# Optimization experiments

Measured on AMD Instinct MI355X. Metric: run time of the kernel, lower is better.

The kernel has to match this reference:

```python
import jax, jax.numpy as jnp
import numpy as np

NUM_HEADS = 10
LN_EPS = 1e-5


def setup_inputs() -> dict:
    key = jax.random.key(0)
    ks = jax.random.split(key, 6)
    N, D = 4096, 640  # in_dim == out_dim required by residual add
    x = jax.random.normal(ks[0], (N, D), dtype=jnp.float32)
    s = 1.0 / np.sqrt(D)
    Wq = jax.random.normal(ks[1], (D, D), dtype=jnp.float32) * s  # torch Linear weight [out,in]
    Wk = jax.random.normal(ks[2], (D, D), dtype=jnp.float32) * s
    Wv = jax.random.normal(ks[3], (D, D), dtype=jnp.float32) * s
    gamma = jnp.ones((D,), dtype=jnp.float32)
    beta = jnp.zeros((D,), dtype=jnp.float32)
    return {"x": x, "Wq": Wq, "Wk": Wk, "Wv": Wv, "gamma": gamma, "beta": beta}


def reference(x, Wq, Wk, Wv, gamma, beta):
    N, D = x.shape
    dk = D // NUM_HEADS
    Q = x @ Wq.T  # [N, D]
    K = x @ Wk.T
    V = x @ Wv.T
    # Faithful to source: raw reshapes (NOT transposes)
    Qh = Q.reshape(NUM_HEADS, N, dk)
    Kh = K.reshape(NUM_HEADS, N, dk).reshape(NUM_HEADS, dk, N)  # torch.reshape, not .mT
    Vh = V.reshape(NUM_HEADS, N, dk)
    # Faithful quirk: scale by sqrt(K.shape[2]) == sqrt(N)
    scale = np.float32(np.sqrt(N))
    wghts = jax.nn.softmax((Qh @ Kh) / scale, axis=-1)  # [H, N, N]
    values = wghts @ Vh  # [H, N, dk]
    values = values.reshape(N, NUM_HEADS * dk)  # raw reshape merge
    values = values + x  # residual
    # LayerNorm(out_dim), biased variance, eps=1e-5
    mean = jnp.mean(values, axis=-1, keepdims=True)
    var = jnp.mean(jnp.square(values - mean), axis=-1, keepdims=True)
    out = (values - mean) * jax.lax.rsqrt(var + LN_EPS) * gamma + beta
    return out
```

## Files before the change

### kernel.cpp

```cpp
#include <hip/hip_runtime.h>
#if __has_include(<hip/hip_fp8.h>)
#include <hip/hip_fp8.h>
#endif


typedef __bf16 bf16x8 __attribute__((ext_vector_type(8)));
typedef __bf16 bf16x4 __attribute__((ext_vector_type(4)));
typedef float  f32x4  __attribute__((ext_vector_type(4)));
typedef unsigned short u16x4 __attribute__((ext_vector_type(4)));
typedef unsigned int   u32x4 __attribute__((ext_vector_type(4)));
typedef long           la64  __attribute__((may_alias));
typedef unsigned int   ua32  __attribute__((may_alias));

#define N_TOK   4096
#define D_MODEL 640
#define DK      64
#define HSLAB   (N_TOK * DK)
#define SQS 0.15014030f

#if __has_builtin(__builtin_amdgcn_exp2f)
#define EXP2(x) __builtin_amdgcn_exp2f(x)
#else
#define EXP2(x) exp2f(x)
#endif

__device__ __forceinline__ void stage16(const void* g, void* lds_uniform) {
    __builtin_amdgcn_global_load_lds(
        (const __attribute__((address_space(1))) unsigned int*)g,
        (__attribute__((address_space(3))) unsigned int*)lds_uniform, 16, 0, 0);
}

__device__ __forceinline__ u16x4 cvt4(f32x4 v) {
    return __builtin_bit_cast(u16x4, __builtin_convertvector(v, bf16x4));
}

__device__ __forceinline__ unsigned int pk_fp8(f32x4 v) {
#if __has_builtin(__builtin_amdgcn_cvt_pk_fp8_f32)
    int r = 0;
    r = __builtin_amdgcn_cvt_pk_fp8_f32(v[0], v[1], r, false);
    r = __builtin_amdgcn_cvt_pk_fp8_f32(v[2], v[3], r, true);
    return (unsigned int)r;
#else
    union { unsigned char b[4]; unsigned int u; } x;
    x.b[0] = __hip_fp8_e4m3(v[0]).__x;
    x.b[1] = __hip_fp8_e4m3(v[1]).__x;
    x.b[2] = __hip_fp8_e4m3(v[2]).__x;
    x.b[3] = __hip_fp8_e4m3(v[3]).__x;
    return x.u;
#endif
}

__global__ __launch_bounds__(256) void cvt_all(const float* __restrict__ x,
                                               const float* __restrict__ w0,
                                               const float* __restrict__ w1,
                                               const float* __restrict__ w2,
                                               unsigned short* __restrict__ xb,
                                               unsigned short* __restrict__ d0,
                                               unsigned short* __restrict__ d1,
                                               unsigned short* __restrict__ d2,
                                               f32x4* __restrict__ ltot4) {
    int i = blockIdx.x * 256 + threadIdx.x;
    if (i >= 962560) { ltot4[i - 962560] = (f32x4){0.f, 0.f, 0.f, 0.f}; return; }
    const float* s; unsigned short* d; int off; float scl = 1.0f;
    if (i < 655360) { s = x; d = xb; off = i; }
    else {
        int j = i - 655360;
        int w = j / 102400; off = j - w * 102400;
        s = (w == 0) ? w0 : (w == 1) ? w1 : w2;
        d = (w == 0) ? d0 : (w == 1) ? d1 : d2;
        if (w < 2) scl = SQS;
    }
    f32x4 v = ((const f32x4*)s)[off];
    v[0] *= scl; v[1] *= scl; v[2] *= scl; v[3] *= scl;
    ((u16x4*)d)[off] = cvt4(v);
}

__global__ __launch_bounds__(256, 2) void gemm_qkv(
    const unsigned short* __restrict__ xb,
    const unsigned short* __restrict__ wq,
    const unsigned short* __restrict__ wk,
    const unsigned short* __restrict__ wv,
    unsigned short* __restrict__ Qo,
    unsigned short* __restrict__ Ko,
    unsigned short* __restrict__ Vo) {
    const int mode = blockIdx.z;
    const unsigned short* W = (mode == 0) ? wq : (mode == 1) ? wk : wv;
    unsigned short*       C = (mode == 0) ? Qo : (mode == 1) ? Ko : Vo;
    const int m0 = blockIdx.y * 128;
    const int n0 = blockIdx.x * 128;

    __shared__ unsigned short As[8192];
    __shared__ unsigned short Bs[8192];

    const int tid  = threadIdx.x;
    const int lane = tid & 63;
    const int wave = tid >> 6;
    const int quad = lane >> 4, l16 = lane & 15;
    const int wm = (wave >> 1) * 64, wn = (wave & 1) * 64;
    const int swz = l16 & 7;

    f32x4 acc[4][4] = {};

    int prow[4], pcol[4], lbase[4];
    for (int j = 0; j < 4; j++) {
        int p = j * 256 + tid;
        prow[j] = p >> 3;
        pcol[j] = ((p & 7) ^ (prow[j] & 7)) * 8;
        lbase[j] = (j * 256 + wave * 64) * 8;
    }

    for (int kt = 0; kt < D_MODEL; kt += 64) {
        __syncthreads();
        for (int j = 0; j < 4; j++) {
            stage16(&xb[(size_t)(m0 + prow[j]) * D_MODEL + kt + pcol[j]], As + lbase[j]);
            stage16(&W [(size_t)(n0 + prow[j]) * D_MODEL + kt + pcol[j]], Bs + lbase[j]);
        }
        __syncthreads();

        for (int s = 0; s < 2; s++) {
            bf16x8 af[4], bfr[4];
            for (int mi = 0; mi < 4; mi++) {
                int row = wm + mi * 16 + l16;
                af[mi] = *(const bf16x8*)&As[row * 64 + (((s << 2) + quad) ^ swz) * 8];
            }
            for (int ni = 0; ni < 4; ni++) {
                int row = wn + ni * 16 + l16;
                bfr[ni] = *(const bf16x8*)&Bs[row * 64 + (((s << 2) + quad) ^ swz) * 8];
            }
            for (int mi = 0; mi < 4; mi++)
                for (int ni = 0; ni < 4; ni++)
                    acc[mi][ni] = __builtin_amdgcn_mfma_f32_16x16x32_bf16(af[mi], bfr[ni], acc[mi][ni], 0, 0, 0);
        }
    }

    for (int mi = 0; mi < 4; mi++)
        for (int ni = 0; ni < 4; ni++) {
            u16x4 cv = cvt4(acc[mi][ni]);
            for (int r = 0; r < 4; r++) {
                int row = m0 + wm + mi * 16 + quad * 4 + r;
                int col = n0 + wn + ni * 16 + l16;
                C[(size_t)row * D_MODEL + col] = cv[r];
            }
        }
}

__global__ __launch_bounds__(256) void transpose_kv(
    const unsigned short* __restrict__ Kn, unsigned char* __restrict__ Kp8,
    const unsigned short* __restrict__ Vn, unsigned char* __restrict__ Vp8,
    const unsigned short* __restrict__ Qn, unsigned char* __restrict__ Qf8) {
    const int z = blockIdx.z;
    const int t = threadIdx.x;

    if (z >= 20) {
        const size_t base = (size_t)(z - 20) * HSLAB + blockIdx.x * 4096 + t * 16;
        bf16x8 v0 = *(const bf16x8*)&Qn[base];
        bf16x8 v1 = *(const bf16x8*)&Qn[base + 8];
        f32x4 a = {(float)v0[0], (float)v0[1], (float)v0[2], (float)v0[3]};
        f32x4 b = {(float)v0[4], (float)v0[5], (float)v0[6], (float)v0[7]};
        f32x4 c = {(float)v1[0], (float)v1[1], (float)v1[2], (float)v1[3]};
        f32x4 d = {(float)v1[4], (float)v1[5], (float)v1[6], (float)v1[7]};
        u32x4 o = {pk_fp8(a), pk_fp8(b), pk_fp8(c), pk_fp8(d)};
        *(u32x4*)&Qf8[base] = o;
        return;
    }

    __shared__ unsigned short T[64][66];
    const unsigned short* src; unsigned char* dst;
    int R, Cc, r0, c0;
    if (z < 10) { src = Kn; dst = Kp8; R = 64;   Cc = 4096; r0 = 0; c0 = blockIdx.x * 64; }
    else        { src = Vn; dst = Vp8; R = 4096; Cc = 64;   r0 = blockIdx.x * 64; c0 = 0; }
    const size_t hb = (size_t)(z % 10) * HSLAB;
    const int rr = t >> 3, c8 = (t & 7) * 8;

    for (int hf = 0; hf < 2; hf++) {
        int r = rr + hf * 32;
        bf16x8 v = *(const bf16x8*)&src[hb + (size_t)(r0 + r) * Cc + c0 + c8];
        for (int j = 0; j < 8; j++) T[r][c8 + j] = ((unsigned short*)&v)[j];
    }
    __syncthreads();
    const bf16x8 zz = {};
    for (int hf = 0; hf < 2; hf++) {
        int r = rr + hf * 32;
        *(bf16x8*)&((unsigned short*)src)[hb + (size_t)(r0 + r) * Cc + c0 + c8] = zz;
    }
    for (int hf = 0; hf < 2; hf++) {
        int oc = rr + hf * 32;
        f32x4 lo, hi;
        for (int j = 0; j < 4; j++) {
            lo[j] = __builtin_bit_cast(float, (unsigned int)T[c8 + j][oc] << 16);
            hi[j] = __builtin_bit_cast(float, (unsigned int)T[c8 + 4 + j][oc] << 16);
        }
        uint2 ov; ov.x = pk_fp8(lo); ov.y = pk_fp8(hi);
        size_t dcol = (z < 10) ? ((size_t)(c0 + oc) * 64 + r0 + c8)
                               : ((size_t)oc * 4096 + r0 + c8);
        *(uint2*)&dst[hb + dcol] = ov;
    }
}

__global__ __launch_bounds__(256, 4) void attn(
    const unsigned char* __restrict__ Qf8,
    const unsigned char* __restrict__ Kp8,
    const unsigned char* __restrict__ Vp8,
    float* __restrict__ vals,
    float* __restrict__ l_tot) {
    const int h  = blockIdx.x >> 5;
    const int qt = blockIdx.x & 31;
    const int ntile = (blockIdx.y == 2) ? 10 : 11;
    const int tile0 = blockIdx.y * 11;
    const int lane = threadIdx.x & 63;
    const int wave = threadIdx.x >> 6;
    const int quad = lane >> 4, l16 = lane & 15;
    const size_t hoff = (size_t)h * HSLAB;

    __shared__ unsigned char sm[32768];
    unsigned char* Kt = sm;
    unsigned char* Vt = sm + 8192;
    unsigned char* Pw = sm + 16384 + wave * 4096;

    const int qbase = qt * 128 + wave * 32;
    long qd[2][2];
    for (int g = 0; g < 2; g++) {
        const unsigned char* qp = Qf8 + hoff + (size_t)(qbase + g * 16 + l16) * 64 + quad * 8;
        qd[g][0] = *(const la64*)(qp);
        qd[g][1] = *(const la64*)(qp + 32);
    }

    f32x4 o[2][4] = {};
    f32x4 ol[2] = {};
    const long ONES8 = 0x3838383838383838L;

    const int cA = wave * 64 + lane, cB = cA + 256;
    const int kKeyA = ((cA >> 5) << 3) + (cA & 7), kCiA = (cA >> 3) & 3;
    const int kKeyB = ((cB >> 5) << 3) + (cB & 7), kCiB = (cB >> 3) & 3;
    const int vDkA  = ((cA >> 6) << 3) + (cA & 7), vCvA = (cA >> 3) & 7;
    const int vDkB  = ((cB >> 6) << 3) + (cB & 7), vCvB = (cB >> 3) & 7;

    const int kfb = (l16 >> 3) * 512 + (quad >> 1) * 128 + (l16 & 7) * 16 + (quad & 1) * 8;
    const int vfb = (l16 >> 3) * 1024 + (quad >> 1) * 128 + (l16 & 7) * 16 + (quad & 1) * 8;

    for (int t = 0; t < ntile; t++) {
        const int keyb = (tile0 + t) << 7;
        __syncthreads();
        stage16(Kp8 + hoff + (size_t)(keyb + kKeyA) * 64 + kCiA * 16, Kt + wave * 1024);
        stage16(Kp8 + hoff + (size_t)(keyb + kKeyB) * 64 + kCiB * 16, Kt + 4096 + wave * 1024);
        stage16(Vp8 + hoff + (size_t)vDkA * N_TOK + keyb + vCvA * 16, Vt + wave * 1024);
        stage16(Vp8 + hoff + (size_t)vDkB * N_TOK + keyb + vCvB * 16, Vt + 4096 + wave * 1024);
        __syncthreads();

        for (int ni = 0; ni < 8; ni++) {
            const unsigned char* kp = Kt + ni * 1024 + kfb;
            long a0 = *(const la64*)(kp);
            long a1 = *(const la64*)(kp + 256);
            for (int g = 0; g < 2; g++) {
                f32x4 s = {};
                s = __builtin_amdgcn_mfma_f32_16x16x32_fp8_fp8(a0, qd[g][0], s, 0, 0, 0);
                s = __builtin_amdgcn_mfma_f32_16x16x32_fp8_fp8(a1, qd[g][1], s, 0, 0, 0);
                f32x4 pv;
                for (int r = 0; r < 4; r++) pv[r] = EXP2(s[r]);
                *(ua32*)(Pw + (ni * 2 + (quad >> 1)) * 256 +
                         (g * 16 + l16) * 8 + (quad & 1) * 4) = pk_fp8(pv);
            }
        }

        __syncthreads();

        for (int ks = 0; ks < 4; ks++) {
            long vf[4];
            for (int nd = 0; nd < 4; nd++)
                vf[nd] = *(const la64*)(Vt + nd * 2048 + ks * 256 + vfb);
            for (int g = 0; g < 2; g++) {
                long pf = *(const la64*)(Pw + (ks * 4 + quad) * 256 + (g * 16 + l16) * 8);
                ol[g] = __builtin_amdgcn_mfma_f32_16x16x32_fp8_fp8(pf, ONES8, ol[g], 0, 0, 0);
                for (int nd = 0; nd < 4; nd++)
                    o[g][nd] = __builtin_amdgcn_mfma_f32_16x16x32_fp8_fp8(pf, vf[nd], o[g][nd], 0, 0, 0);
            }
        }
    }

    if (l16 == 0)
        for (int g = 0; g < 2; g++)
            for (int r = 0; r < 4; r++)
                atomicAdd(&l_tot[(h << 12) + qbase + g * 16 + quad * 4 + r], ol[g][r]);

    for (int g = 0; g < 2; g++)
        for (int nd = 0; nd < 4; nd++)
            for (int r = 0; r < 4; r++) {
                int q = qbase + g * 16 + quad * 4 + r;
                atomicAdd(&vals[hoff + (size_t)q * DK + nd * 16 + l16], o[g][nd][r]);
            }
}

__global__ __launch_bounds__(256) void ln_kernel(
    const float* __restrict__ vals, const float* __restrict__ l_tot,
    const float* __restrict__ x,
    const float* __restrict__ gamma, const float* __restrict__ beta,
    float* __restrict__ out) {
    const int wave = threadIdx.x >> 6, lane = threadIdx.x & 63;
    const int row  = blockIdx.x * 4 + wave;
    const float* v  = vals + (size_t)row * D_MODEL;
    const float* xr = x    + (size_t)row * D_MODEL;

    float t[10];
    float s = 0.f;
    for (int i = 0; i < 10; i++) {
        float linv = 1.0f / l_tot[row * 10 + i];
        t[i] = v[lane + i * 64] * linv + xr[lane + i * 64];
        s += t[i];
    }
    for (int off = 32; off; off >>= 1) s += __shfl_xor(s, off, 64);
    float mean = s * (1.0f / 640.0f);
    float s2 = 0.f;
    for (int i = 0; i < 10; i++) { float d = t[i] - mean; s2 += d * d; }
    for (int off = 32; off; off >>= 1) s2 += __shfl_xor(s2, off, 64);
    float inv = rsqrtf(s2 * (1.0f / 640.0f) + 1e-5f);

    float* orow = out + (size_t)row * D_MODEL;
    for (int i = 0; i < 10; i++) {
        int c = lane + i * 64;
        orow[c] = (t[i] - mean) * inv * gamma[c] + beta[c];
    }
}

extern "C" void kernel_launch(void* const* d_in, const int* in_sizes, int n_in,
                              void* d_out, int out_size, void* d_ws, size_t ws_size,
                              hipStream_t stream) {
    const float* x     = (const float*)d_in[0];
    const float* Wq    = (const float*)d_in[1];
    const float* Wk    = (const float*)d_in[2];
    const float* Wv    = (const float*)d_in[3];
    const float* gamma = (const float*)d_in[4];
    const float* beta  = (const float*)d_in[5];
    float* out = (float*)d_out;

    char* ws = (char*)d_ws;
    unsigned short* xb  = (unsigned short*)(ws);
    unsigned char*  Qf8 = (unsigned char*)(ws);
    unsigned short* wqb = (unsigned short*)(ws + 5242880);
    unsigned short* wkb = (unsigned short*)(ws + 6062080);
    unsigned short* wvb = (unsigned short*)(ws + 6881280);
    unsigned short* Qn  = (unsigned short*)(ws + 7700480);
    unsigned char*  Kp8 = (unsigned char*)(ws + 12943360);
    unsigned char*  Vp8 = (unsigned char*)(ws + 18186240);
    unsigned short* Kn  = (unsigned short*)(ws + 23429120);
    unsigned short* Vn  = (unsigned short*)(ws + 28672000);
    float*          vals  = (float*)(ws + 23429120);
    float*          l_tot = (float*)(ws + 33914880);

    cvt_all<<<3800, 256, 0, stream>>>(x, Wq, Wk, Wv, xb, wqb, wkb, wvb,
                                      (f32x4*)l_tot);

    gemm_qkv<<<dim3(5, 32, 3), 256, 0, stream>>>(xb, wqb, wkb, wvb, Qn, Kn, Vn);

    transpose_kv<<<dim3(64, 1, 30), 256, 0, stream>>>(Kn, Kp8, Vn, Vp8, Qn, Qf8);

    attn<<<dim3(320, 3), 256, 0, stream>>>(Qf8, Kp8, Vp8, vals, l_tot);
    ln_kernel<<<1024, 256, 0, stream>>>(vals, l_tot, x, gamma, beta, out);
}
```

Measured before the change: 160.2 us.

## Keep P in registers and use bf16 PV MFMA, fusing Q fp8 conversion into attention

```diff
diff --git a/kernel.cpp b/kernel.cpp
--- a/kernel.cpp
+++ b/kernel.cpp
@@ -8,9 +8,8 @@
 typedef __bf16 bf16x4 __attribute__((ext_vector_type(4)));
 typedef float  f32x4  __attribute__((ext_vector_type(4)));
 typedef unsigned short u16x4 __attribute__((ext_vector_type(4)));
-typedef unsigned int   u32x4 __attribute__((ext_vector_type(4)));
+typedef short          s16x4 __attribute__((ext_vector_type(4)));
 typedef long           la64  __attribute__((may_alias));
-typedef unsigned int   ua32  __attribute__((may_alias));
 
 #define N_TOK   4096
 #define D_MODEL 640
@@ -48,6 +47,10 @@
     x.b[3] = __hip_fp8_e4m3(v[3]).__x;
     return x.u;
 #endif
+}
+
+__device__ __forceinline__ f32x4 mfma16bf(s16x4 a, s16x4 b, f32x4 c) {
+    return __builtin_amdgcn_mfma_f32_16x16x16bf16_1k(a, b, c, 0, 0, 0);
 }
 
 __global__ __launch_bounds__(256) void cvt_all(const float* __restrict__ x,
@@ -146,29 +149,15 @@
 
 __global__ __launch_bounds__(256) void transpose_kv(
     const unsigned short* __restrict__ Kn, unsigned char* __restrict__ Kp8,
-    const unsigned short* __restrict__ Vn, unsigned char* __restrict__ Vp8,
-    const unsigned short* __restrict__ Qn, unsigned char* __restrict__ Qf8) {
+    const unsigned short* __restrict__ Vn, unsigned short* __restrict__ Vpb) {
     const int z = blockIdx.z;
     const int t = threadIdx.x;
 
-    if (z >= 20) {
-        const size_t base = (size_t)(z - 20) * HSLAB + blockIdx.x * 4096 + t * 16;
-        bf16x8 v0 = *(const bf16x8*)&Qn[base];
-        bf16x8 v1 = *(const bf16x8*)&Qn[base + 8];
-        f32x4 a = {(float)v0[0], (float)v0[1], (float)v0[2], (float)v0[3]};
-        f32x4 b = {(float)v0[4], (float)v0[5], (float)v0[6], (float)v0[7]};
-        f32x4 c = {(float)v1[0], (float)v1[1], (float)v1[2], (float)v1[3]};
-        f32x4 d = {(float)v1[4], (float)v1[5], (float)v1[6], (float)v1[7]};
-        u32x4 o = {pk_fp8(a), pk_fp8(b), pk_fp8(c), pk_fp8(d)};
-        *(u32x4*)&Qf8[base] = o;
-        return;
-    }
-
     __shared__ unsigned short T[64][66];
-    const unsigned short* src; unsigned char* dst;
-    int R, Cc, r0, c0;
-    if (z < 10) { src = Kn; dst = Kp8; R = 64;   Cc = 4096; r0 = 0; c0 = blockIdx.x * 64; }
-    else        { src = Vn; dst = Vp8; R = 4096; Cc = 64;   r0 = blockIdx.x * 64; c0 = 0; }
+    const unsigned short* src;
+    int Cc, r0, c0;
+    if (z < 10) { src = Kn; Cc = 4096; r0 = 0; c0 = blockIdx.x * 64; }
+    else        { src = Vn; Cc = 64;   r0 = blockIdx.x * 64; c0 = 0; }
     const size_t hb = (size_t)(z % 10) * HSLAB;
     const int rr = t >> 3, c8 = (t & 7) * 8;
 
@@ -183,24 +172,31 @@
         int r = rr + hf * 32;
         *(bf16x8*)&((unsigned short*)src)[hb + (size_t)(r0 + r) * Cc + c0 + c8] = zz;
     }
-    for (int hf = 0; hf < 2; hf++) {
-        int oc = rr + hf * 32;
-        f32x4 lo, hi;
-        for (int j = 0; j < 4; j++) {
-            lo[j] = __builtin_bit_cast(float, (unsigned int)T[c8 + j][oc] << 16);
-            hi[j] = __builtin_bit_cast(float, (unsigned int)T[c8 + 4 + j][oc] << 16);
-        }
-        uint2 ov; ov.x = pk_fp8(lo); ov.y = pk_fp8(hi);
-        size_t dcol = (z < 10) ? ((size_t)(c0 + oc) * 64 + r0 + c8)
-                               : ((size_t)oc * 4096 + r0 + c8);
-        *(uint2*)&dst[hb + dcol] = ov;
-    }
-}
-
-__global__ __launch_bounds__(256, 4) void attn(
-    const unsigned char* __restrict__ Qf8,
-    const unsigned char* __restrict__ Kp8,
-    const unsigned char* __restrict__ Vp8,
+    if (z < 10) {
+        for (int hf = 0; hf < 2; hf++) {
+            int oc = rr + hf * 32;
+            f32x4 lo, hi;
+            for (int j = 0; j < 4; j++) {
+                lo[j] = __builtin_bit_cast(float, (unsigned int)T[c8 + j][oc] << 16);
+                hi[j] = __builtin_bit_cast(float, (unsigned int)T[c8 + 4 + j][oc] << 16);
+            }
+            uint2 ov; ov.x = pk_fp8(lo); ov.y = pk_fp8(hi);
+            *(uint2*)&Kp8[hb + (size_t)(c0 + oc) * 64 + r0 + c8] = ov;
+        }
+    } else {
+        for (int hf = 0; hf < 2; hf++) {
+            int oc = rr + hf * 32;
+            unsigned short v[8];
+            for (int j = 0; j < 8; j++) v[j] = T[c8 + j][oc];
+            *(bf16x8*)&Vpb[hb + (size_t)oc * 4096 + r0 + c8] = *(bf16x8*)v;
+        }
+    }
+}
+
+__global__ __launch_bounds__(256, 5) void attn(
+    const unsigned short* __restrict__ Qn,
+    const unsigned char*  __restrict__ Kp8,
+    const unsigned short* __restrict__ Vpb,
     float* __restrict__ vals,
     float* __restrict__ l_tot) {
     const int h  = blockIdx.x >> 5;
@@ -212,67 +208,61 @@
     const int quad = lane >> 4, l16 = lane & 15;
     const size_t hoff = (size_t)h * HSLAB;
 
-    __shared__ unsigned char sm[32768];
-    unsigned char* Kt = sm;
-    unsigned char* Vt = sm + 8192;
-    unsigned char* Pw = sm + 16384 + wave * 4096;
+    __shared__ unsigned char Kt[8192];
+    __shared__ unsigned char Vt[32768 - 8192];
 
     const int qbase = qt * 128 + wave * 32;
     long qd[2][2];
-    for (int g = 0; g < 2; g++) {
-        const unsigned char* qp = Qf8 + hoff + (size_t)(qbase + g * 16 + l16) * 64 + quad * 8;
-        qd[g][0] = *(const la64*)(qp);
-        qd[g][1] = *(const la64*)(qp + 32);
-    }
+    for (int g = 0; g < 2; g++)
+        for (int s = 0; s < 2; s++) {
+            bf16x8 qv = *(const bf16x8*)&Qn[hoff + (size_t)(qbase + g * 16 + l16) * DK + s * 32 + quad * 8];
+            f32x4 lo = {(float)qv[0], (float)qv[1], (float)qv[2], (float)qv[3]};
+            f32x4 hi = {(float)qv[4], (float)qv[5], (float)qv[6], (float)qv[7]};
+            uint2 t2; t2.x = pk_fp8(lo); t2.y = pk_fp8(hi);
+            qd[g][s] = __builtin_bit_cast(long, t2);
+        }
 
     f32x4 o[2][4] = {};
     f32x4 ol[2] = {};
-    const long ONES8 = 0x3838383838383838L;
-
-    const int cA = wave * 64 + lane, cB = cA + 256;
-    const int kKeyA = ((cA >> 5) << 3) + (cA & 7), kCiA = (cA >> 3) & 3;
-    const int kKeyB = ((cB >> 5) << 3) + (cB & 7), kCiB = (cB >> 3) & 3;
-    const int vDkA  = ((cA >> 6) << 3) + (cA & 7), vCvA = (cA >> 3) & 7;
-    const int vDkB  = ((cB >> 6) << 3) + (cB & 7), vCvB = (cB >> 3) & 7;
-
-    const int kfb = (l16 >> 3) * 512 + (quad >> 1) * 128 + (l16 & 7) * 16 + (quad & 1) * 8;
-    const int vfb = (l16 >> 3) * 1024 + (quad >> 1) * 128 + (l16 & 7) * 16 + (quad & 1) * 8;
+    const s16x4 ONES4 = (s16x4)(short)0x3F80;
+
+    const int l = lane;
+    const int kKey0 = wave * 32 + ((l >> 1) & 15);
+    const int kCi   = (((l >> 5) & 1) << 1) | (l & 1);
+    const int vDk   = wave * 16 + ((l >> 1) & 15);
+    const int vKc   = (((l >> 5) & 1) << 1) | (l & 1);
+
+    const int kfb = l16 * 32 + (quad >> 1) * 16 + (quad & 1) * 8;
+    const int vfb = l16 * 32 + quad * 8;
 
     for (int t = 0; t < ntile; t++) {
         const int keyb = (tile0 + t) << 7;
         __syncthreads();
-        stage16(Kp8 + hoff + (size_t)(keyb + kKeyA) * 64 + kCiA * 16, Kt + wave * 1024);
-        stage16(Kp8 + hoff + (size_t)(keyb + kKeyB) * 64 + kCiB * 16, Kt + 4096 + wave * 1024);
-        stage16(Vp8 + hoff + (size_t)vDkA * N_TOK + keyb + vCvA * 16, Vt + wave * 1024);
-        stage16(Vp8 + hoff + (size_t)vDkB * N_TOK + keyb + vCvB * 16, Vt + 4096 + wave * 1024);
+        stage16(Kp8 + hoff + (size_t)(keyb + kKey0) * 64 + kCi * 16, Kt + wave * 2048);
+        stage16(Kp8 + hoff + (size_t)(keyb + kKey0 + 16) * 64 + kCi * 16, Kt + wave * 2048 + 1024);
+        for (int j = 0; j < 4; j++)
+            stage16(Vpb + hoff + (size_t)vDk * 4096 + keyb + (j * 4 + vKc) * 8,
+                    Vt + wave * 4096 + j * 1024);
         __syncthreads();
 
         for (int ni = 0; ni < 8; ni++) {
             const unsigned char* kp = Kt + ni * 1024 + kfb;
             long a0 = *(const la64*)(kp);
-            long a1 = *(const la64*)(kp + 256);
+            long a1 = *(const la64*)(kp + 512);
+            s16x4 vb[4];
+            for (int nd = 0; nd < 4; nd++)
+                vb[nd] = __builtin_bit_cast(s16x4,
+                    *(const la64*)(Vt + nd * 4096 + ni * 512 + vfb));
             for (int g = 0; g < 2; g++) {
                 f32x4 s = {};
                 s = __builtin_amdgcn_mfma_f32_16x16x32_fp8_fp8(a0, qd[g][0], s, 0, 0, 0);
                 s = __builtin_amdgcn_mfma_f32_16x16x32_fp8_fp8(a1, qd[g][1], s, 0, 0, 0);
                 f32x4 pv;
                 for (int r = 0; r < 4; r++) pv[r] = EXP2(s[r]);
-                *(ua32*)(Pw + (ni * 2 + (quad >> 1)) * 256 +
-                         (g * 16 + l16) * 8 + (quad & 1) * 4) = pk_fp8(pv);
-            }
-        }
-
-        __syncthreads();
-
-        for (int ks = 0; ks < 4; ks++) {
-            long vf[4];
-            for (int nd = 0; nd < 4; nd++)
-                vf[nd] = *(const la64*)(Vt + nd * 2048 + ks * 256 + vfb);
-            for (int g = 0; g < 2; g++) {
-                long pf = *(const la64*)(Pw + (ks * 4 + quad) * 256 + (g * 16 + l16) * 8);
-                ol[g] = __builtin_amdgcn_mfma_f32_16x16x32_fp8_fp8(pf, ONES8, ol[g], 0, 0, 0);
+                s16x4 A = __builtin_bit_cast(s16x4, cvt4(pv));
+                ol[g] = mfma16bf(A, ONES4, ol[g]);
                 for (int nd = 0; nd < 4; nd++)
-                    o[g][nd] = __builtin_amdgcn_mfma_f32_16x16x32_fp8_fp8(pf, vf[nd], o[g][nd], 0, 0, 0);
+                    o[g][nd] = mfma16bf(A, vb[nd], o[g][nd]);
             }
         }
     }
@@ -334,13 +324,12 @@
 
     char* ws = (char*)d_ws;
     unsigned short* xb  = (unsigned short*)(ws);
-    unsigned char*  Qf8 = (unsigned char*)(ws);
+    unsigned char*  Kp8 = (unsigned char*)(ws);
     unsigned short* wqb = (unsigned short*)(ws + 5242880);
     unsigned short* wkb = (unsigned short*)(ws + 6062080);
     unsigned short* wvb = (unsigned short*)(ws + 6881280);
     unsigned short* Qn  = (unsigned short*)(ws + 7700480);
-    unsigned char*  Kp8 = (unsigned char*)(ws + 12943360);
-    unsigned char*  Vp8 = (unsigned char*)(ws + 18186240);
+    unsigned short* Vpb = (unsigned short*)(ws + 12943360);
     unsigned short* Kn  = (unsigned short*)(ws + 23429120);
     unsigned short* Vn  = (unsigned short*)(ws + 28672000);
     float*          vals  = (float*)(ws + 23429120);
@@ -351,8 +340,8 @@
 
     gemm_qkv<<<dim3(5, 32, 3), 256, 0, stream>>>(xb, wqb, wkb, wvb, Qn, Kn, Vn);
 
-    transpose_kv<<<dim3(64, 1, 30), 256, 0, stream>>>(Kn, Kp8, Vn, Vp8, Qn, Qf8);
-
-    attn<<<dim3(320, 3), 256, 0, stream>>>(Qf8, Kp8, Vp8, vals, l_tot);
+    transpose_kv<<<dim3(64, 1, 20), 256, 0, stream>>>(Kn, Kp8, Vn, Vpb);
+
+    attn<<<dim3(320, 3), 256, 0, stream>>>(Qn, Kp8, Vpb, vals, l_tot);
     ln_kernel<<<1024, 256, 0, stream>>>(vals, l_tot, x, gamma, beta, out);
 }
```

Result: slower. 186.3 us (+16.3%).
